# Performance work log

Measured on AMD Instinct MI355X. Metric: run time of the kernel, lower is better.

Reference implementation:

```python
import jax, jax.numpy as jnp
import numpy as np

N, M, S = 1536, 1536, 3
POS = ((-1, -1), (-1, 0), (0, -1))  # match, X (gap in y), Y (gap in x)
NEG_INF = -1.0e8  # matches the torch implementation's neg_inf literal


def _hmm_forward(theta):
    """Smoothed-max (softmax operator) forward DP over a 3-state pair HMM.

    theta: (N, M, S, S) combined transition+emission potentials.
    V[i, j, s] = logsumexp_k( V[i+di_s, j+dj_s, k] + theta[i-1, j-1, s, k] )
    Vt = logsumexp_k V[N, M, k]
    Implemented as a row scan (dependence on previous row) with an inner
    column scan (dependence on V[i, j-1] via the Y state).
    """
    n, m, s, _ = theta.shape
    # V[0, :] border: V[0,0] = 0 (all states), rest -inf
    init_row = jnp.full((m + 1, s), NEG_INF, theta.dtype).at[0].set(0.0)
    v_border = jnp.full((s,), NEG_INF, theta.dtype)  # V[i, 0]

    def col_step(v_left, inputs):
        diag, up, th = inputs  # V[i-1,j-1](S,), V[i-1,j](S,), theta[i-1,j-1](S,S)
        # row s of src = predecessor V-vector selected by pos[s]
        src = jnp.stack([diag if p == (-1, -1) else (up if p == (-1, 0) else v_left)
                         for p in POS])          # (S, S)
        v_new = jax.nn.logsumexp(src + th, axis=-1)  # (S,)
        return v_new, v_new

    def row_step(prev_row, theta_row):
        # prev_row: (M+1, S) = V[i-1, :]; theta_row: (M, S, S)
        _, vals = jax.lax.scan(col_step, v_border,
                               (prev_row[:-1], prev_row[1:], theta_row))
        new_row = jnp.concatenate([v_border[None], vals], axis=0)  # (M+1, S)
        return new_row, None

    last_row, _ = jax.lax.scan(row_step, init_row, theta)
    # terminal smoothed max over V[N, M]
    return jax.nn.logsumexp(last_row[m])


def setup_inputs() -> dict:
    key = jax.random.key(0)
    theta = jax.random.normal(key, (N, M, S, S), dtype=jnp.float32)
    return {"theta": theta}


def reference(theta):
    return _hmm_forward(theta)
```

## Files before the change

### kernel.cpp

```cpp
#include <hip/hip_runtime.h>


#define MM 1536
#define HH 64
#define NB 24
#define U  8
#define NBLK 200
#define LOG2E 1.4426950408889634f
#define LN2   0.6931471805599453f
#define NEG2  (-1.4426950408889634e8f)

#define LDS_TH  4608
#define LDS_FD  9216
#define LDS_FDB 64

typedef float f32x4 __attribute__((ext_vector_type(4)));
typedef float f32x2 __attribute__((ext_vector_type(2)));

template <int BYTES>
__device__ __forceinline__ void gl_lds(const float* g, float* l) {
    auto* gp = (const __attribute__((address_space(1))) float*)(g);
    auto* lp = (__attribute__((address_space(3))) float*)(l);
    if constexpr (BYTES == 16) __builtin_amdgcn_global_load_lds(gp, lp, 16, 0, 0);
    else                       __builtin_amdgcn_global_load_lds(gp, lp, 4, 0, 0);
}

__device__ __forceinline__ float shup1(float x) {
    int xi = __builtin_bit_cast(int, x);
    int r  = __builtin_amdgcn_update_dpp(xi, xi, 0x138, 0xF, 0xF, false);
    return __builtin_bit_cast(float, r);
}

__device__ __forceinline__ float lse3_2(float a, float b, float c) {
    float mx = fmaxf(fmaxf(a, b), c);
    float mn = fminf(fminf(a, b), c);
    float md = __builtin_amdgcn_fmed3f(a, b, c);
    return mx + __builtin_amdgcn_logf(1.0f + __builtin_amdgcn_exp2f(mn - mx)
                                           + __builtin_amdgcn_exp2f(md - mx));
}

__global__ void init_progress_kernel(int* progress) {
    if (threadIdx.x < NB) progress[threadIdx.x] = -1;
}

__global__ __launch_bounds__(64, 1)
void hmm_fwd_kernel(const float* __restrict__ theta, float* __restrict__ out,
                    float* __restrict__ bottom, int* __restrict__ progress)
{
    __shared__ __align__(16) float smem[2 * LDS_TH + 2 * LDS_FDB];

    const int b    = blockIdx.x;
    const int lane = threadIdx.x;
    const float* __restrict__ thp = theta + (size_t)(b * HH + lane) * (MM * 9);
    const float* __restrict__ bsrc =
        bottom + (size_t)(b > 0 ? b - 1 : 0) * ((MM + 1) * 3);
    float* __restrict__ bdst = bottom + (size_t)b * ((MM + 1) * 3);

    float d0, d1, d2, l0, l1, l2, s0, s1, s2, res0, res1, res2;
    d0 = d1 = d2 = (b == 0 && lane == 0) ? 0.0f : NEG2;
    l0 = l1 = l2 = NEG2;
    s0 = s1 = s2 = NEG2;
    res0 = res1 = res2 = NEG2;

    const int fidx = lane < 24 ? lane : 23;
    const int fk   = fidx / 3;
    const int fr   = fidx - fk * 3;

    auto issue_block = [&](int tb, int nbuf) {
        #pragma unroll
        for (int k = 0; k < U; ++k) {
            int c = tb + k - lane;
            c = c < 0 ? 0 : (c > MM - 1 ? MM - 1 : c);
            const float* g = thp + (size_t)c * 9;
            float* base = &smem[nbuf * LDS_TH + k * 576];
            gl_lds<16>(g,     base);
            gl_lds<16>(g + 4, base + 256);
            gl_lds<4 >(g + 8, base + 512);
        }
        if (b > 0) {
            int jn = tb + fk + 1; if (jn > MM) jn = MM;
            gl_lds<4>(bsrc + (size_t)jn * 3 + fr, &smem[LDS_FD + nbuf * LDS_FDB]);
        }
    };

    if (b > 0) {
        while (__hip_atomic_load(&progress[b - 1], __ATOMIC_ACQUIRE,
                                 __HIP_MEMORY_SCOPE_AGENT) < 24)
            __builtin_amdgcn_s_sleep(2);
    }

    issue_block(0, 0);
    asm volatile("s_waitcnt vmcnt(0)" ::: "memory");
    __builtin_amdgcn_sched_barrier(0);

    auto block_body = [&](int T, int cb, bool mlo, bool mhi) {
        const int t0 = T * U;
        const int nbuf = cb ^ 1;

        if (b > 0 && T > 0 && (T & 1) == 0) {
            int need = t0 + 24; if (need > MM) need = MM;
            while (__hip_atomic_load(&progress[b - 1], __ATOMIC_ACQUIRE,
                                     __HIP_MEMORY_SCOPE_AGENT) < need)
                __builtin_amdgcn_s_sleep(2);
        }

        if (b < NB - 1) asm volatile("s_waitcnt vmcnt(16)" ::: "memory");
        else            asm volatile("s_waitcnt vmcnt(0)"  ::: "memory");

        issue_block(t0 + U, nbuf);

        if (b < NB - 1 && lane == HH - 1) {
            int val = t0 - 71;
            if (val >= 1) {
                if (val > MM) val = MM;
                __hip_atomic_store(&progress[b], val, __ATOMIC_RELAXED,
                                   __HIP_MEMORY_SCOPE_AGENT);
            }
        }
        __builtin_amdgcn_sched_barrier(0);

        const float* base  = &smem[cb * LDS_TH];
        const float* fbase = &smem[LDS_FD + cb * LDS_FDB];
        f32x4 q0 = *(const f32x4*)(base + lane * 4);
        f32x4 q1 = *(const f32x4*)(base + 256 + lane * 4);
        float s8 = base[512 + lane];
        float f0 = NEG2, f1 = NEG2, f2 = NEG2;
        if (b > 0) { f0 = fbase[0]; f1 = fbase[1]; f2 = fbase[2]; }

        #pragma unroll
        for (int k = 0; k < U; ++k) {
            f32x4 q0n, q1n; float s8n, f0n = NEG2, f1n = NEG2, f2n = NEG2;
            if (k < U - 1) {
                const float* cp = base + (k + 1) * 576;
                q0n = *(const f32x4*)(cp + lane * 4);
                q1n = *(const f32x4*)(cp + 256 + lane * 4);
                s8n = cp[512 + lane];
                if (b > 0) {
                    f0n = fbase[(k + 1) * 3];
                    f1n = fbase[(k + 1) * 3 + 1];
                    f2n = fbase[(k + 1) * 3 + 2];
                }
            }

            const int c = t0 + k - lane;
            bool act = true;
            if (mlo || mhi) act = ((unsigned)c < (unsigned)MM);

            float u0 = (lane == 0) ? f0 : s0;
            float u1 = (lane == 0) ? f1 : s1;
            float u2 = (lane == 0) ? f2 : s2;

            float aa0 = fmaf(q0.x, LOG2E, d0);
            float aa1 = fmaf(q0.y, LOG2E, d1);
            float aa2 = fmaf(q0.z, LOG2E, d2);
            float bb0 = fmaf(q0.w, LOG2E, u0);
            float bb1 = fmaf(q1.x, LOG2E, u1);
            float bb2 = fmaf(q1.y, LOG2E, u2);
            float cc0 = fmaf(q1.z, LOG2E, l0);
            float cc1 = fmaf(q1.w, LOG2E, l1);
            float cc2 = fmaf(s8,   LOG2E, l2);

            float n0 = lse3_2(aa0, aa1, aa2);
            float n1 = lse3_2(bb0, bb1, bb2);
            float n2 = lse3_2(cc0, cc1, cc2);
            if (mlo || mhi) {
                n0 = act ? n0 : NEG2;
                n1 = act ? n1 : NEG2;
                n2 = act ? n2 : NEG2;
            }

            if (b < NB - 1 && lane == HH - 1) {
                int j = c + 1;
                if (mlo || mhi) j = act ? c + 1 : 0;
                float* sa = bdst + (size_t)j * 3;
                f32x2 p01; p01.x = n0; p01.y = n1;
                asm volatile("global_store_dwordx2 %0, %1, off sc1"
                             :: "v"(sa), "v"(p01) : "memory");
                asm volatile("global_store_dword %0, %1, off offset:8 sc1"
                             :: "v"(sa), "v"(n2) : "memory");
            }

            if (mhi) {
                const bool fin = (c == MM - 1);
                res0 = fin ? n0 : res0;
                res1 = fin ? n1 : res1;
                res2 = fin ? n2 : res2;
            }

            d0 = u0; d1 = u1; d2 = u2;
            s0 = shup1(n0);
            s1 = shup1(n1);
            s2 = shup1(n2);
            l0 = n0; l1 = n1; l2 = n2;

            if (k < U - 1) {
                q0 = q0n; q1 = q1n; s8 = s8n;
                f0 = f0n; f1 = f1n; f2 = f2n;
            }
        }
    };

    for (int T = 0;   T < 8;    ++T) block_body(T, T & 1, true,  false);
    for (int T = 8;   T < 192;  ++T) block_body(T, T & 1, false, false);
    for (int T = 192; T < NBLK; ++T) block_body(T, T & 1, false, true);

    if (b < NB - 1 && lane == HH - 1) {
        asm volatile("s_waitcnt vmcnt(0)" ::: "memory");
        __hip_atomic_store(&progress[b], MM, __ATOMIC_RELEASE,
                           __HIP_MEMORY_SCOPE_AGENT);
    }

    if (b == NB - 1 && lane == HH - 1)
        out[0] = LN2 * lse3_2(res0, res1, res2);
}

extern "C" void kernel_launch(void* const* d_in, const int* in_sizes, int n_in,
                              void* d_out, int out_size, void* d_ws, size_t ws_size,
                              hipStream_t stream)
{
    const float* theta = (const float*)d_in[0];
    float* out = (float*)d_out;

    float* bottom   = (float*)d_ws;
    int*   progress = (int*)((char*)d_ws +
                             (size_t)NB * (MM + 1) * 3 * sizeof(float));

    init_progress_kernel<<<1, 64, 0, stream>>>(progress);
    hmm_fwd_kernel<<<NB, HH, 0, stream>>>(theta, out, bottom, progress);
}
```

Measured before the change: 1.079 ms.

## Pre-skew theta into anti-diagonal-contiguous layout before the wavefront DP kernel

Adds a parallel pre-pass that rearranges theta so that each anti-diagonal step's 64 lanes × 9 values sit in one contiguous 576-float chunk. The serial DP kernel can then fill LDS with 18 coalesced 16-byte global-to-LDS loads per block instead of strided per-lane gathers. The goal is to cut load latency and issue cost on the latency-bound critical path. In exchange it adds a full read and write of about 90MB of theta through workspace, and it falls back to the old path if the workspace is too small.

```diff
diff --git a/kernel.cpp b/kernel.cpp
--- a/kernel.cpp
+++ b/kernel.cpp
@@ -6,6 +6,7 @@
 #define NB 24
 #define U  8
 #define NBLK 200
+#define NSTEP 1608
 #define LOG2E 1.4426950408889634f
 #define LN2   0.6931471805599453f
 #define NEG2  (-1.4426950408889634e8f)
@@ -43,15 +44,45 @@
     if (threadIdx.x < NB) progress[threadIdx.x] = -1;
 }
 
+__global__ __launch_bounds__(256)
+void skew_kernel(const float* __restrict__ theta, float* __restrict__ skew)
+{
+    const int wid  = blockIdx.x * 4 + (threadIdx.x >> 6);
+    const int lane = threadIdx.x & 63;
+    const int b = wid / NSTEP;
+    const int t = wid - b * NSTEP;
+
+    const int c = t - lane;
+    float v[9];
+    if ((unsigned)c < (unsigned)MM) {
+        const float* g = theta + ((size_t)(b * HH + lane) * MM + c) * 9;
+        __builtin_memcpy(&v[0], g, 36);
+    } else {
+        #pragma unroll
+        for (int i = 0; i < 9; ++i) v[i] = 0.0f;
+    }
+
+    float* o = skew + (size_t)(b * NSTEP + t) * 576;
+    f32x4 a; a.x = v[0]; a.y = v[1]; a.z = v[2]; a.w = v[3];
+    f32x4 q; q.x = v[4]; q.y = v[5]; q.z = v[6]; q.w = v[7];
+    *(f32x4*)(o + lane * 4)       = a;
+    *(f32x4*)(o + 256 + lane * 4) = q;
+    o[512 + lane] = v[8];
+}
+
+template <bool SKEW>
 __global__ __launch_bounds__(64, 1)
-void hmm_fwd_kernel(const float* __restrict__ theta, float* __restrict__ out,
+void hmm_fwd_kernel(const float* __restrict__ src, float* __restrict__ out,
                     float* __restrict__ bottom, int* __restrict__ progress)
 {
     __shared__ __align__(16) float smem[2 * LDS_TH + 2 * LDS_FDB];
 
     const int b    = blockIdx.x;
     const int lane = threadIdx.x;
-    const float* __restrict__ thp = theta + (size_t)(b * HH + lane) * (MM * 9);
+    const float* __restrict__ thp =
+        SKEW ? nullptr : src + (size_t)(b * HH + lane) * (MM * 9);
+    const float* __restrict__ skp =
+        SKEW ? src + (size_t)b * NSTEP * 576 : nullptr;
     const float* __restrict__ bsrc =
         bottom + (size_t)(b > 0 ? b - 1 : 0) * ((MM + 1) * 3);
     float* __restrict__ bdst = bottom + (size_t)b * ((MM + 1) * 3);
@@ -67,15 +98,23 @@
     const int fr   = fidx - fk * 3;
 
     auto issue_block = [&](int tb, int nbuf) {
-        #pragma unroll
-        for (int k = 0; k < U; ++k) {
-            int c = tb + k - lane;
-            c = c < 0 ? 0 : (c > MM - 1 ? MM - 1 : c);
-            const float* g = thp + (size_t)c * 9;
-            float* base = &smem[nbuf * LDS_TH + k * 576];
-            gl_lds<16>(g,     base);
-            gl_lds<16>(g + 4, base + 256);
-            gl_lds<4 >(g + 8, base + 512);
+        if constexpr (SKEW) {
+            const float* g0 = skp + (size_t)tb * 576 + lane * 4;
+            float* l0_ = &smem[nbuf * LDS_TH];
+            #pragma unroll
+            for (int d = 0; d < 18; ++d)
+                gl_lds<16>(g0 + d * 256, l0_ + d * 256);
+        } else {
+            #pragma unroll
+            for (int k = 0; k < U; ++k) {
+                int c = tb + k - lane;
+                c = c < 0 ? 0 : (c > MM - 1 ? MM - 1 : c);
+                const float* g = thp + (size_t)c * 9;
+                float* base = &smem[nbuf * LDS_TH + k * 576];
+                gl_lds<16>(g,     base);
+                gl_lds<16>(g + 4, base + 256);
+                gl_lds<4 >(g + 8, base + 512);
+            }
         }
         if (b > 0) {
             int jn = tb + fk + 1; if (jn > MM) jn = MM;
@@ -221,10 +260,21 @@
     const float* theta = (const float*)d_in[0];
     float* out = (float*)d_out;
 
-    float* bottom   = (float*)d_ws;
-    int*   progress = (int*)((char*)d_ws +
-                             (size_t)NB * (MM + 1) * 3 * sizeof(float));
-
-    init_progress_kernel<<<1, 64, 0, stream>>>(progress);
-    hmm_fwd_kernel<<<NB, HH, 0, stream>>>(theta, out, bottom, progress);
-}
+    const size_t skew_fl = (size_t)NB * NSTEP * 576;
+    const size_t bot_fl  = (size_t)NB * (MM + 1) * 3;
+    const size_t need    = (skew_fl + bot_fl) * sizeof(float) + NB * sizeof(int);
+
+    if (ws_size >= need) {
+        float* skew     = (float*)d_ws;
+        float* bottom   = skew + skew_fl;
+        int*   progress = (int*)(bottom + bot_fl);
+        init_progress_kernel<<<1, 64, 0, stream>>>(progress);
+        skew_kernel<<<(NB * NSTEP) / 4, 256, 0, stream>>>(theta, skew);
+        hmm_fwd_kernel<true><<<NB, HH, 0, stream>>>(skew, out, bottom, progress);
+    } else {
+        float* bottom   = (float*)d_ws;
+        int*   progress = (int*)((char*)d_ws + bot_fl * sizeof(float));
+        init_progress_kernel<<<1, 64, 0, stream>>>(progress);
+        hmm_fwd_kernel<false><<<NB, HH, 0, stream>>>(theta, out, bottom, progress);
+    }
+}
```

After: 1.040 ms. -3.6%, faster.
